# Kernel tuning notes

Measured on AMD Instinct MI355X. Metric: run time of the kernel, lower is better.

## Reference

```python
import jax, jax.numpy as jnp
import numpy as np

B, N_C, N_F = 2, 16384, 65536          # batch, coarse nodes, fine (up_nodes)
C_IN, C_OUT = 128, 128
E_C, E_F = 65536, 262144               # coarse / fine edge counts


def _mlp_params(key, cin, cout):
    # 2-layer MLP (Linear-ReLU-Linear) + LayerNorm, torch default uniform init
    k1, k2 = jax.random.split(key)
    s1 = 1.0 / np.sqrt(2 * cin)
    s2 = 1.0 / np.sqrt(cout)
    W1 = jax.random.uniform(k1, (2 * cin, cout), minval=-s1, maxval=s1, dtype=jnp.float32)
    W2 = jax.random.uniform(k2, (cout, cout), minval=-s2, maxval=s2, dtype=jnp.float32)
    return (W1, jnp.zeros((cout,), jnp.float32), W2, jnp.zeros((cout,), jnp.float32),
            jnp.ones((cout,), jnp.float32), jnp.zeros((cout,), jnp.float32))


def setup_inputs() -> dict:
    key = jax.random.key(0)
    rng = np.random.default_rng(0)
    x = jax.random.normal(jax.random.fold_in(key, 1), (B, N_C, C_IN), dtype=jnp.float32)
    # sorted unique unpool indices (m_id)
    idx = jnp.asarray(np.sort(rng.choice(N_F, N_C, replace=False)).astype(np.int64))
    ei_c = jnp.asarray(rng.integers(0, N_C, size=(2, E_C)).astype(np.int64))
    ei_f = jnp.asarray(rng.integers(0, N_F, size=(2, E_F)).astype(np.int64))
    d = {"x": x, "idx": idx, "ei_c": ei_c, "ei_f": ei_f}
    for pre, k, cin, cout in (("s", 2, C_IN, C_OUT), ("a", 3, C_IN, C_OUT // 2), ("b", 4, C_OUT // 2, C_OUT)):
        W1, b1, W2, b2, g, bt = _mlp_params(jax.random.fold_in(key, k), cin, cout)
        d.update({pre + "W1": W1, pre + "b1": b1, pre + "W2": W2, pre + "b2": b2, pre + "g": g, pre + "bt": bt})
    return d


def _unpool(x, idx, n):
    # scatter coarse features into a zero-filled fine array (Unpool module)
    return jnp.zeros((x.shape[0], n, x.shape[-1]), x.dtype).at[:, idx].set(x)


def _edgeconv(x, ei, W1, b1, W2, b2, g, bt, n):
    # EdgeConv: aggregate_sum over edges of MLP([x_i, x_j - x_i]) + LayerNorm
    src, dst = ei[0], ei[1]
    xd = x[:, dst]                                   # [B,E,cin] gather at target
    feat = jnp.concatenate([xd, x[:, src] - xd], axis=-1)  # [B,E,2*cin]
    h = jax.nn.relu(feat @ W1 + b1) @ W2 + b2        # [B,E,cout]
    mu = jnp.mean(h, axis=-1, keepdims=True)
    var = jnp.var(h, axis=-1, keepdims=True)
    h = (h - mu) * jax.lax.rsqrt(var + 1e-5) * g + bt
    return jax.vmap(lambda hb: jax.ops.segment_sum(hb, dst, num_segments=n))(h)


def reference(x, idx, ei_c, ei_f,
              sW1, sb1, sW2, sb2, sg, sbt,
              aW1, ab1, aW2, ab2, ag, abt,
              bW1, bb1, bW2, bb2, bg, bbt):
    # skip branch: unpool then EdgeConv cin->cout on fine graph
    skip = _edgeconv(_unpool(x, idx, N_F), ei_f, sW1, sb1, sW2, sb2, sg, sbt, N_F)
    # main branch: EdgeConv cin->cout/2 on coarse, unpool, EdgeConv cout/2->cout on fine
    h = _edgeconv(x, ei_c, aW1, ab1, aW2, ab2, ag, abt, N_C)
    h = _edgeconv(_unpool(h, idx, N_F), ei_f, bW1, bb1, bW2, bb2, bg, bbt, N_F)
    return jax.nn.leaky_relu(h + skip, 0.01)
```

## Files before the change

### kernel.cpp

```cpp
#include <hip/hip_runtime.h>

typedef _Float16 half8  __attribute__((ext_vector_type(8)));
typedef _Float16 half4v __attribute__((ext_vector_type(4)));
typedef _Float16 half2v __attribute__((ext_vector_type(2)));
typedef float    f32x4  __attribute__((ext_vector_type(4)));
typedef float    f32x2  __attribute__((ext_vector_type(2)));
typedef int      i32x4  __attribute__((ext_vector_type(4)));

#define NB 2
#define N_C 16384
#define N_F 65536
#define E_C 65536
#define E_F 262144

#define INV4  ((size_t)N_F / 4)
#define CNT4  ((size_t)(N_F + N_C) / 4)

__global__ void clear_small(int* __restrict__ inv, int* __restrict__ cnt) {
    size_t i = (size_t)blockIdx.x * 256 + threadIdx.x;
    const i32x4 z = {0, 0, 0, 0};
    const i32x4 m1 = {-1, -1, -1, -1};
    if (i < INV4) ((i32x4*)inv)[i] = m1;
    else if (i < INV4 + CNT4) ((i32x4*)cnt)[i - INV4] = z;
}

__device__ inline void swizzle_dev(const float* __restrict__ W, _Float16* __restrict__ Ws,
                                   int N, int o) {
    int j = o & 7;
    int lane = (o >> 3) & 63;
    int frag = o >> 9;
    int ntiles = N >> 4;
    int nt = frag % ntiles;
    int kt = frag / ntiles;
    int k = kt * 32 + (lane >> 4) * 8 + j;
    int n = nt * 16 + (lane & 15);
    Ws[o] = (_Float16)W[k * N + n];
}

__device__ inline void swz_node(const float* __restrict__ W, _Float16* __restrict__ Ws,
                                int CIN, int COUT, int o) {
    int j = o & 7;
    int lane = (o >> 3) & 63;
    int frag = o >> 9;
    int N2 = 2 * COUT;
    int ntiles = N2 >> 4;
    int nt = frag % ntiles;
    int kt = frag / ntiles;
    int k = kt * 32 + (lane >> 4) * 8 + j;
    int n = nt * 16 + (lane & 15);
    float v = (n < COUT) ? W[k * COUT + n] - W[(k + CIN) * COUT + n]
                         : W[(k + CIN) * COUT + (n - COUT)];
    Ws[o] = (_Float16)v;
}

__global__ void setup_all(const int* __restrict__ idx, int* __restrict__ inv,
                          const float* sW1, const float* sW2, const float* aW1,
                          const float* aW2, const float* bW1, const float* bW2,
                          const float* sb1, const float* ab1, const float* bb1,
                          _Float16* sW1n, _Float16* sW2s, _Float16* aW1n,
                          _Float16* aW2s, _Float16* bW1n, _Float16* bW2s,
                          _Float16* b1h,
                          const int* __restrict__ ei_f, const int* __restrict__ ei_c,
                          int* __restrict__ cnt) {
    const int bb = blockIdx.x, t = threadIdx.x;
    if (bb < 64) {
        int i = bb * 256 + t;
        inv[idx[i]] = i;
    } else if (bb < 192) {
        swz_node(sW1, sW1n, 128, 128, (bb - 64) * 256 + t);
    } else if (bb < 256) {
        swizzle_dev(sW2, sW2s, 128, (bb - 192) * 256 + t);
    } else if (bb < 320) {
        swz_node(aW1, aW1n, 128, 64, (bb - 256) * 256 + t);
    } else if (bb < 336) {
        swizzle_dev(aW2, aW2s, 64, (bb - 320) * 256 + t);
    } else if (bb < 400) {
        swz_node(bW1, bW1n, 64, 128, (bb - 336) * 256 + t);
    } else if (bb < 464) {
        swizzle_dev(bW2, bW2s, 128, (bb - 400) * 256 + t);
    } else if (bb < 466) {
        int i = (bb - 464) * 256 + t;
        if (i < 128) b1h[i] = (_Float16)sb1[i];
        else if (i < 192) b1h[i] = (_Float16)ab1[i - 128];
        else if (i < 320) b1h[i] = (_Float16)bb1[i - 192];
    } else if (bb < 1490) {
        int e = (bb - 466) * 256 + t;
        atomicAdd(&cnt[ei_f[E_F + e]], 1);
    } else {
        int e = (bb - 1490) * 256 + t;
        atomicAdd(&cnt[N_F + ei_c[E_C + e]], 1);
    }
}

__global__ void scan1(const int* __restrict__ cnt, int* __restrict__ csum) {
    __shared__ int red[4];
    int v = cnt[blockIdx.x * 256 + threadIdx.x];
    #pragma unroll
    for (int off = 32; off >= 1; off >>= 1) v += __shfl_xor(v, off, 64);
    if ((threadIdx.x & 63) == 0) red[threadIdx.x >> 6] = v;
    __syncthreads();
    if (threadIdx.x == 0) csum[blockIdx.x] = red[0] + red[1] + red[2] + red[3];
}

__global__ void scan2(const int* __restrict__ csum, int* __restrict__ cbase) {
    __shared__ int buf[256];
    const int t = threadIdx.x;
    int v = csum[t];
    buf[t] = v;
    __syncthreads();
    for (int off = 1; off < 256; off <<= 1) {
        int u = (t >= off) ? buf[t - off] : 0;
        __syncthreads();
        buf[t] += u;
        __syncthreads();
    }
    cbase[t] = buf[t] - v;
    __syncthreads();
    int v2 = (t < 64) ? csum[256 + t] : 0;
    buf[t] = v2;
    __syncthreads();
    for (int off = 1; off < 64; off <<= 1) {
        int u = (t >= off) ? buf[t - off] : 0;
        __syncthreads();
        buf[t] += u;
        __syncthreads();
    }
    if (t < 64) cbase[256 + t] = buf[t] - v2;
}

__global__ void scan3(const int* __restrict__ cnt, const int* __restrict__ cbase,
                      int* __restrict__ cursor) {
    __shared__ int buf[256];
    const int t = threadIdx.x, bb = blockIdx.x;
    int v = cnt[bb * 256 + t];
    buf[t] = v;
    __syncthreads();
    for (int off = 1; off < 256; off <<= 1) {
        int u = (t >= off) ? buf[t - off] : 0;
        __syncthreads();
        buf[t] += u;
        __syncthreads();
    }
    cursor[bb * 256 + t] = cbase[bb] + buf[t] - v;
}

__global__ void scatter2(const int* __restrict__ ei_f, const int* __restrict__ ei_c,
                         int* __restrict__ cursor,
                         int* __restrict__ perm_f, int* __restrict__ perm_c) {
    const int bb = blockIdx.x, t = threadIdx.x;
    if (bb < 1024) {
        int e = bb * 256 + t;
        int d = ei_f[E_F + e];
        int p = atomicAdd(&cursor[d], 1);
        perm_f[p] = e;
    } else {
        int e = (bb - 1024) * 256 + t;
        int d = ei_c[E_C + e];
        int p = atomicAdd(&cursor[N_F + d], 1);
        perm_c[p] = e;
    }
}

__global__ void zero_flag(const int* __restrict__ cnt, const int* __restrict__ cursor,
                          unsigned char* __restrict__ flagF,
                          float* __restrict__ out, float* __restrict__ h_a) {
    const int d = blockIdx.x * 256 + threadIdx.x;
    const f32x4 z = {0.f, 0.f, 0.f, 0.f};
    if (d < N_F) {
        const int deg = cnt[d];
        const int end = cursor[d];
        const int start = end - deg;
        const bool pred = (deg == 0) || ((start >> 5) != ((end - 1) >> 5));
        flagF[d] = pred ? 1 : 0;
        if (pred) {
            f32x4* r0 = (f32x4*)(out + (size_t)d * 128);
            f32x4* r1 = (f32x4*)(out + ((size_t)N_F + d) * 128);
            #pragma unroll
            for (int i = 0; i < 32; ++i) { r0[i] = z; r1[i] = z; }
        }
    } else if (d < N_F + N_C) {
        const int dc = d - N_F;
        const int deg = cnt[d];
        const int end = cursor[d];
        const int start = end - deg;
        const bool pred = (deg == 0) || ((start >> 4) != ((end - 1) >> 4));
        if (pred) {
            f32x4* r0 = (f32x4*)(h_a + (size_t)dc * 64);
            f32x4* r1 = (f32x4*)(h_a + ((size_t)N_C + dc) * 64);
            #pragma unroll
            for (int i = 0; i < 16; ++i) { r0[i] = z; r1[i] = z; }
        }
    }
}

template <int CIN, int COUT>
__launch_bounds__(256, 4) __global__
void node_gemm(const float* __restrict__ x, const _Float16* __restrict__ W1n,
               const float* __restrict__ b1, _Float16* __restrict__ P) {
    constexpr int N2 = 2 * COUT;
    constexpr int FP = CIN + 8;
    constexpr int P2 = N2 + 8;
    constexpr int NPW = N2 / 4;
    constexpr int NT = NPW / 16;
    constexpr int RH = (64 * FP > 64 * P2) ? 64 * FP : 64 * P2;

    __shared__ __align__(16) _Float16 L[RH];
    const int t = threadIdx.x;
    const size_t r0 = (size_t)blockIdx.x * 64;

    {
        const int m = t >> 2, l4 = t & 3;
        const float* src = x + (r0 + m) * CIN + l4 * (CIN / 4);
        #pragma unroll
        for (int i = 0; i < CIN / 16; ++i) {
            f32x4 v = *(const f32x4*)(src + i * 4);
            half4v h;
            #pragma unroll
            for (int c = 0; c < 4; ++c) h[c] = (_Float16)v[c];
            *(half4v*)(L + m * FP + l4 * (CIN / 4) + i * 4) = h;
        }
    }
    __syncthreads();

    const int wv = t >> 6, lane = t & 63;
    const int q = lane >> 4, lm = lane & 15;
    const int n0 = wv * NPW;
    const f32x4 zero4 = {0.f, 0.f, 0.f, 0.f};

    f32x4 acc[4][NT];
    #pragma unroll
    for (int mt = 0; mt < 4; ++mt)
        #pragma unroll
        for (int nt = 0; nt < NT; ++nt) acc[mt][nt] = zero4;

    #pragma unroll
    for (int kt = 0; kt < CIN / 32; ++kt) {
        half8 a[4];
        #pragma unroll
        for (int mt = 0; mt < 4; ++mt)
            a[mt] = *(const half8*)(L + (mt * 16 + lm) * FP + kt * 32 + q * 8);
        #pragma unroll
        for (int nt = 0; nt < NT; ++nt) {
            half8 bf = *(const half8*)(W1n + ((size_t)(kt * (N2 / 16) + wv * NT + nt) * 64 + lane) * 8);
            #pragma unroll
            for (int mt = 0; mt < 4; ++mt)
                acc[mt][nt] = __builtin_amdgcn_mfma_f32_16x16x32_f16(a[mt], bf, acc[mt][nt], 0, 0, 0);
        }
    }
    __syncthreads();

    #pragma unroll
    for (int nt = 0; nt < NT; ++nt) {
        const int col = n0 + nt * 16 + lm;
        const float bv = (col < COUT) ? b1[col] : 0.f;
        #pragma unroll
        for (int mt = 0; mt < 4; ++mt)
            #pragma unroll
            for (int r = 0; r < 4; ++r)
                L[(mt * 16 + q * 4 + r) * P2 + col] = (_Float16)(acc[mt][nt][r] + bv);
    }
    __syncthreads();

    constexpr int CH = 64 * N2 / 8;
    for (int i = t; i < CH; i += 256) {
        int row = i / (N2 / 8), c8 = i % (N2 / 8);
        *(half8*)(P + (r0 + row) * N2 + c8 * 8) = *(const half8*)(L + row * P2 + c8 * 8);
    }
}

__device__ inline half8 relu8(half8 h) {
#if __has_builtin(__builtin_elementwise_max)
    half8 z = {};
    return __builtin_elementwise_max(h, z);
#else
    #pragma unroll
    for (int i = 0; i < 8; ++i) h[i] = h[i] > (_Float16)0 ? h[i] : (_Float16)0;
    return h;
#endif
}

template <int COUT, bool FRESH>
__launch_bounds__(256, 8) __global__
void edge2_mfma(const _Float16* __restrict__ P, int ps,
                const int* __restrict__ inv,
                const int* __restrict__ ei, const int* __restrict__ perm, int E,
                const _Float16* __restrict__ W2s, const float* __restrict__ b2,
                const float* __restrict__ g, const float* __restrict__ bt,
                const _Float16* __restrict__ b1h,
                float* __restrict__ dest, int bs_out) {
    constexpr int HPITCH = COUT + 8;
    constexpr int NPW = COUT / 4;
    constexpr int NT = NPW / 16;

    __shared__ __align__(16) _Float16 region[64 * HPITCH];
    __shared__ int dstl[64];
    __shared__ int dpnL[2];
    __shared__ float muL[64];
    __shared__ float rsL[64];

    _Float16* h1L = region;
    _Float16* vnL = region;

    const int t = threadIdx.x;
    const int eb = blockIdx.x * 64;
    const int b = eb / E;
    const int e0 = eb - b * E;

    {
        if (t == 0) dpnL[0] = (e0 > 0) ? ei[E + perm[e0 - 1]] : -2;
        else if (t == 1) dpnL[1] = (e0 + 64 < E) ? ei[E + perm[e0 + 64]] : -2;
        const int m = t >> 2, l4 = t & 3;
        const int edge = perm[e0 + m];
        int s = ei[edge], d = ei[E + edge];
        if (l4 == 0) dstl[m] = d;
        int si = s, di = d;
        if (inv) { si = inv[s]; di = inv[d]; }
        const _Float16* pb = P + (size_t)b * ps;
        const _Float16* ub = (di >= 0) ? pb + (size_t)di * (2 * COUT) : b1h;
        const _Float16* vb = pb + (size_t)(si >= 0 ? si : 0) * (2 * COUT) + COUT;
        constexpr int CPT = COUT / 4;
        const int c0 = l4 * CPT;
        #pragma unroll
        for (int i = 0; i < CPT / 8; ++i) {
            half8 u = *(const half8*)(ub + c0 + i * 8);
            half8 v = {};
            if (si >= 0) v = *(const half8*)(vb + c0 + i * 8);
            *(half8*)(h1L + m * HPITCH + c0 + i * 8) = relu8(u + v);
        }
    }
    __syncthreads();

    const int wv = t >> 6, lane = t & 63;
    const int q = lane >> 4, lm = lane & 15;
    const int n0 = wv * NPW;
    const f32x4 zero4 = {0.f, 0.f, 0.f, 0.f};

    f32x4 acc[4][NT];
    #pragma unroll
    for (int mt = 0; mt < 4; ++mt)
        #pragma unroll
        for (int nt = 0; nt < NT; ++nt) acc[mt][nt] = zero4;

    #pragma unroll
    for (int kt = 0; kt < COUT / 32; ++kt) {
        half8 a[4];
        #pragma unroll
        for (int mt = 0; mt < 4; ++mt)
            a[mt] = *(const half8*)(h1L + (mt * 16 + lm) * HPITCH + kt * 32 + q * 8);
        #pragma unroll
        for (int nt = 0; nt < NT; ++nt) {
            half8 bf = *(const half8*)(W2s + ((size_t)(kt * (COUT / 16) + wv * NT + nt) * 64 + lane) * 8);
            #pragma unroll
            for (int mt = 0; mt < 4; ++mt)
                acc[mt][nt] = __builtin_amdgcn_mfma_f32_16x16x32_f16(a[mt], bf, acc[mt][nt], 0, 0, 0);
        }
    }
    __syncthreads();

    #pragma unroll
    for (int nt = 0; nt < NT; ++nt) {
        const float b2v = b2[n0 + nt * 16 + lm];
        #pragma unroll
        for (int mt = 0; mt < 4; ++mt)
            #pragma unroll
            for (int r = 0; r < 4; ++r)
                vnL[(mt * 16 + q * 4 + r) * HPITCH + n0 + nt * 16 + lm] =
                    (_Float16)(acc[mt][nt][r] + b2v);
    }
    __syncthreads();

    {
        const int m = t >> 2, p = t & 3;
        constexpr int CPT = COUT / 4;
        float s = 0.f, s2 = 0.f;
        #pragma unroll
        for (int c = 0; c < CPT / 8; ++c) {
            half8 h8 = *(const half8*)(vnL + m * HPITCH + p * CPT + c * 8);
            #pragma unroll
            for (int j = 0; j < 8; ++j) {
                float v = (float)h8[j];
                s += v;
                s2 += v * v;
            }
        }
        s += __shfl_xor(s, 1, 64);  s2 += __shfl_xor(s2, 1, 64);
        s += __shfl_xor(s, 2, 64);  s2 += __shfl_xor(s2, 2, 64);
        if (p == 0) {
            float mu = s * (1.f / COUT);
            muL[m] = mu;
            rsL[m] = rsqrtf(s2 * (1.f / COUT) - mu * mu + 1e-5f);
        }
    }
    __syncthreads();

    {
        constexpr int CG = COUT / 64;
        constexpr int W  = 4 / CG;
        constexpr int RW = 64 / W;
        const int wv2 = t >> 6, l2 = t & 63;
        const int cg = wv2 % CG;
        const int h  = wv2 / CG;
        const int c  = cg * 64 + l2;
        const int r0 = h * RW;
        const float gv = g[c], bv = bt[c];
        float* const ob = dest + (size_t)b * bs_out + c;
        int dcur = dstl[r0];
        const int dprev = (r0 == 0) ? dpnL[0] : dstl[r0 - 1];
        bool bflag = (dcur == dprev);
        float rs = 0.f;
        #pragma unroll
        for (int i = 0; i < RW; ++i) {
            const int m = r0 + i;
            const float v = (float)vnL[m * HPITCH + c];
            rs += (v - muL[m]) * rsL[m] * gv + bv;
            const int dnxt = (i == RW - 1)
                               ? ((r0 + RW == 64) ? dpnL[1] : dstl[r0 + RW])
                               : dstl[m + 1];
            if (dnxt != dcur) {
                if (!FRESH || bflag) atomicAdd(ob + (size_t)dcur * COUT, rs);
                else ob[(size_t)dcur * COUT] = rs;
                rs = 0.f; dcur = dnxt; bflag = false;
            } else if (i == RW - 1) {
                atomicAdd(ob + (size_t)dcur * COUT, rs);
            }
        }
    }
}

__launch_bounds__(256, 4) __global__
void edge2_dual(const _Float16* __restrict__ Ps, const _Float16* __restrict__ Pb,
                const int* __restrict__ inv,
                const int* __restrict__ ei, const int* __restrict__ perm,
                const _Float16* __restrict__ W2sS, const float* __restrict__ b2s,
                const float* __restrict__ gS, const float* __restrict__ btS,
                const _Float16* __restrict__ W2sB, const float* __restrict__ b2b,
                const float* __restrict__ gB, const float* __restrict__ btB,
                const _Float16* __restrict__ b1hS, const _Float16* __restrict__ b1hB,
                float* __restrict__ out) {
    constexpr int E = E_F;
    constexpr int HP = 136;

    __shared__ __align__(16) _Float16 regS[64 * HP];
    __shared__ __align__(16) _Float16 regB[64 * HP];
    __shared__ int dstl[64];
    __shared__ int dpn[2];
    __shared__ float muS[64], rsS[64], muB[64], rsB[64];

    const int t = threadIdx.x;
    const int eb = blockIdx.x * 64;
    const int b = eb / E;
    const int e0 = eb - b * E;

    {
        if (t == 0) dpn[0] = (e0 > 0) ? ei[E + perm[e0 - 1]] : -2;
        else if (t == 1) dpn[1] = (e0 + 64 < E) ? ei[E + perm[e0 + 64]] : -2;
        const int m = t >> 2, l4 = t & 3;
        const int edge = perm[e0 + m];
        const int s = ei[edge], d = ei[E + edge];
        if (l4 == 0) dstl[m] = d;
        const int si = inv[s], di = inv[d];
        const size_t pofs = (size_t)b * ((size_t)N_C * 256);
        const _Float16* ubS = (di >= 0) ? Ps + pofs + (size_t)di * 256 : b1hS;
        const _Float16* ubB = (di >= 0) ? Pb + pofs + (size_t)di * 256 : b1hB;
        const size_t so = (size_t)(si >= 0 ? si : 0) * 256 + 128;
        const _Float16* vbS = Ps + pofs + so;
        const _Float16* vbB = Pb + pofs + so;
        const int c0 = l4 * 32;
        #pragma unroll
        for (int i = 0; i < 4; ++i) {
            half8 uS = *(const half8*)(ubS + c0 + i * 8);
            half8 uB = *(const half8*)(ubB + c0 + i * 8);
            half8 vS = {}, vB = {};
            if (si >= 0) {
                vS = *(const half8*)(vbS + c0 + i * 8);
                vB = *(const half8*)(vbB + c0 + i * 8);
            }
            *(half8*)(regS + m * HP + c0 + i * 8) = relu8(uS + vS);
            *(half8*)(regB + m * HP + c0 + i * 8) = relu8(uB + vB);
        }
    }
    __syncthreads();

    const int wv = t >> 6, lane = t & 63;
    const int q = lane >> 4, lm = lane & 15;
    const int n0 = wv * 32;
    const f32x4 zero4 = {0.f, 0.f, 0.f, 0.f};

    f32x4 accS[4][2], accB[4][2];
    #pragma unroll
    for (int mt = 0; mt < 4; ++mt)
        #pragma unroll
        for (int nt = 0; nt < 2; ++nt) { accS[mt][nt] = zero4; accB[mt][nt] = zero4; }

    #pragma unroll
    for (int kt = 0; kt < 4; ++kt) {
        half8 aS[4], aB[4];
        #pragma unroll
        for (int mt = 0; mt < 4; ++mt) {
            aS[mt] = *(const half8*)(regS + (mt * 16 + lm) * HP + kt * 32 + q * 8);
            aB[mt] = *(const half8*)(regB + (mt * 16 + lm) * HP + kt * 32 + q * 8);
        }
        #pragma unroll
        for (int nt = 0; nt < 2; ++nt) {
            half8 bS = *(const half8*)(W2sS + ((size_t)(kt * 8 + wv * 2 + nt) * 64 + lane) * 8);
            half8 bB = *(const half8*)(W2sB + ((size_t)(kt * 8 + wv * 2 + nt) * 64 + lane) * 8);
            #pragma unroll
            for (int mt = 0; mt < 4; ++mt) {
                accS[mt][nt] = __builtin_amdgcn_mfma_f32_16x16x32_f16(aS[mt], bS, accS[mt][nt], 0, 0, 0);
                accB[mt][nt] = __builtin_amdgcn_mfma_f32_16x16x32_f16(aB[mt], bB, accB[mt][nt], 0, 0, 0);
            }
        }
    }
    __syncthreads();

    #pragma unroll
    for (int nt = 0; nt < 2; ++nt) {
        const float b2vS = b2s[n0 + nt * 16 + lm];
        const float b2vB = b2b[n0 + nt * 16 + lm];
        #pragma unroll
        for (int mt = 0; mt < 4; ++mt)
            #pragma unroll
            for (int r = 0; r < 4; ++r) {
                const int row = mt * 16 + q * 4 + r;
                regS[row * HP + n0 + nt * 16 + lm] = (_Float16)(accS[mt][nt][r] + b2vS);
                regB[row * HP + n0 + nt * 16 + lm] = (_Float16)(accB[mt][nt][r] + b2vB);
            }
    }
    __syncthreads();

    {
        const int m = t >> 2, p = t & 3;
        float sS = 0.f, s2S = 0.f, sB = 0.f, s2B = 0.f;
        #pragma unroll
        for (int c8 = 0; c8 < 4; ++c8) {
            half8 hS = *(const half8*)(regS + m * HP + p * 32 + c8 * 8);
            half8 hB = *(const half8*)(regB + m * HP + p * 32 + c8 * 8);
            #pragma unroll
            for (int j = 0; j < 8; ++j) {
                float a = (float)hS[j]; sS += a; s2S += a * a;
                float c = (float)hB[j]; sB += c; s2B += c * c;
            }
        }
        sS += __shfl_xor(sS, 1, 64);  s2S += __shfl_xor(s2S, 1, 64);
        sS += __shfl_xor(sS, 2, 64);  s2S += __shfl_xor(s2S, 2, 64);
        sB += __shfl_xor(sB, 1, 64);  s2B += __shfl_xor(s2B, 1, 64);
        sB += __shfl_xor(sB, 2, 64);  s2B += __shfl_xor(s2B, 2, 64);
        if (p == 0) {
            float mS = sS * (1.f / 128.f);
            muS[m] = mS;
            rsS[m] = rsqrtf(s2S * (1.f / 128.f) - mS * mS + 1e-5f);
            float mB = sB * (1.f / 128.f);
            muB[m] = mB;
            rsB[m] = rsqrtf(s2B * (1.f / 128.f) - mB * mB + 1e-5f);
        }
    }
    __syncthreads();

    {
        const int wv2 = t >> 6, l2 = t & 63;
        const int cg = wv2 & 1;
        const int h  = wv2 >> 1;
        const int c  = cg * 64 + l2;
        const int r0 = h * 32;
        const float gs = gS[c], bs_ = btS[c];
        const float gb = gB[c], bb_ = btB[c];
        float* const ob = out + (size_t)b * ((size_t)N_F * 128) + c;
        int dcur = dstl[r0];
        const int dprev = (r0 == 0) ? dpn[0] : dstl[r0 - 1];
        bool bflag = (dcur == dprev);
        float rs = 0.f;
        #pragma unroll
        for (int i = 0; i < 32; ++i) {
            const int m = r0 + i;
            const float vs_ = (float)regS[m * HP + c];
            const float vb_ = (float)regB[m * HP + c];
            rs += (vs_ - muS[m]) * rsS[m] * gs + bs_
                + (vb_ - muB[m]) * rsB[m] * gb + bb_;
            const int dnxt = (i == 31)
                               ? ((r0 + 32 == 64) ? dpn[1] : dstl[r0 + 32])
                               : dstl[m + 1];
            if (dnxt != dcur) {
                if (bflag) {
                    atomicAdd(ob + (size_t)dcur * 128, rs);
                } else {
                    float v = rs > 0.f ? rs : 0.01f * rs;
                    ob[(size_t)dcur * 128] = v;
                }
                rs = 0.f; dcur = dnxt; bflag = false;
            } else if (i == 31) {
                atomicAdd(ob + (size_t)dcur * 128, rs);
            }
        }
    }
}

__global__ void leaky_fix(float* __restrict__ out, const unsigned char* __restrict__ flagF) {
    const size_t i = (size_t)blockIdx.x * 256 + threadIdx.x;
    if (i >= (size_t)NB * N_F * 32) return;
    const int d = (int)((i >> 5) & (N_F - 1));
    if (!flagF[d]) return;
    f32x4 v = ((f32x4*)out)[i];
    #pragma unroll
    for (int c = 0; c < 4; ++c) v[c] = v[c] > 0.f ? v[c] : 0.01f * v[c];
    ((f32x4*)out)[i] = v;
}

extern "C" void kernel_launch(void* const* d_in, const int* in_sizes, int n_in,
                              void* d_out, int out_size, void* d_ws, size_t ws_size,
                              hipStream_t stream) {
    const float* x    = (const float*)d_in[0];
    const int*   idx  = (const int*)d_in[1];
    const int*   ei_c = (const int*)d_in[2];
    const int*   ei_f = (const int*)d_in[3];
    const float* sW1 = (const float*)d_in[4];
    const float* sb1 = (const float*)d_in[5];
    const float* sW2 = (const float*)d_in[6];
    const float* sb2 = (const float*)d_in[7];
    const float* sg  = (const float*)d_in[8];
    const float* sbt = (const float*)d_in[9];
    const float* aW1 = (const float*)d_in[10];
    const float* ab1 = (const float*)d_in[11];
    const float* aW2 = (const float*)d_in[12];
    const float* ab2 = (const float*)d_in[13];
    const float* ag  = (const float*)d_in[14];
    const float* abt = (const float*)d_in[15];
    const float* bW1 = (const float*)d_in[16];
    const float* bb1 = (const float*)d_in[17];
    const float* bW2 = (const float*)d_in[18];
    const float* bb2 = (const float*)d_in[19];
    const float* bg  = (const float*)d_in[20];
    const float* bbt = (const float*)d_in[21];

    float* out = (float*)d_out;

    char* ws = (char*)d_ws;
    int*   inv    = (int*)ws;                                ws += (size_t)N_F * 4;
    float* h_a    = (float*)ws;                              ws += (size_t)NB * N_C * 64 * 4;
    int*   perm_f = (int*)ws;                                ws += (size_t)E_F * 4;
    int*   perm_c = (int*)ws;                                ws += (size_t)E_C * 4;
    int*   cnt    = (int*)ws;                                ws += (size_t)(N_F + N_C) * 4;
    int*   cursor = (int*)ws;                                ws += (size_t)(N_F + N_C) * 4;
    int*   csum   = (int*)ws;                                ws += 320 * 4;
    int*   cbase  = (int*)ws;                                ws += 320 * 4;
    _Float16* sW1n = (_Float16*)ws;                          ws += (size_t)128 * 256 * 2;
    _Float16* sW2s = (_Float16*)ws;                          ws += (size_t)128 * 128 * 2;
    _Float16* aW1n = (_Float16*)ws;                          ws += (size_t)128 * 128 * 2;
    _Float16* aW2s = (_Float16*)ws;                          ws += (size_t)64 * 64 * 2;
    _Float16* bW1n = (_Float16*)ws;                          ws += (size_t)64 * 256 * 2;
    _Float16* bW2s = (_Float16*)ws;                          ws += (size_t)128 * 128 * 2;
    _Float16* b1h  = (_Float16*)ws;                          ws += 1024;
    unsigned char* flagF = (unsigned char*)ws;               ws += (size_t)N_F;
    _Float16* P_s  = (_Float16*)ws;                          ws += (size_t)NB * N_C * 256 * 2;
    _Float16* P_a  = (_Float16*)ws;                          ws += (size_t)NB * N_C * 128 * 2;
    _Float16* P_b  = (_Float16*)ws;                          ws += (size_t)NB * N_C * 256 * 2;

    clear_small<<<(int)((INV4 + CNT4 + 255) / 256), 256, 0, stream>>>(inv, cnt);

    setup_all<<<1746, 256, 0, stream>>>(idx, inv, sW1, sW2, aW1, aW2, bW1, bW2,
                                        sb1, ab1, bb1,
                                        sW1n, sW2s, aW1n, aW2s, bW1n, bW2s, b1h,
                                        ei_f, ei_c, cnt);

    scan1<<<320, 256, 0, stream>>>(cnt, csum);
    scan2<<<1, 256, 0, stream>>>(csum, cbase);
    scan3<<<320, 256, 0, stream>>>(cnt, cbase, cursor);
    scatter2<<<1280, 256, 0, stream>>>(ei_f, ei_c, cursor, perm_f, perm_c);

    zero_flag<<<(N_F + N_C) / 256, 256, 0, stream>>>(cnt, cursor, flagF, out, h_a);

    node_gemm<128, 128><<<NB * N_C / 64, 256, 0, stream>>>(x, sW1n, sb1, P_s);
    node_gemm<128, 64><<<NB * N_C / 64, 256, 0, stream>>>(x, aW1n, ab1, P_a);

    edge2_mfma<64, true><<<NB * E_C / 64, 256, 0, stream>>>(
        P_a, N_C * 128, nullptr, ei_c, perm_c, E_C, aW2s, ab2, ag, abt, b1h + 128, h_a, N_C * 64);

    node_gemm<64, 128><<<NB * N_C / 64, 256, 0, stream>>>(h_a, bW1n, bb1, P_b);

    edge2_dual<<<NB * E_F / 64, 256, 0, stream>>>(
        P_s, P_b, inv, ei_f, perm_f,
        sW2s, sb2, sg, sbt,
        bW2s, bb2, bg, bbt,
        b1h, b1h + 192, out);

    leaky_fix<<<(int)(((size_t)NB * N_F * 32 + 255) / 256), 256, 0, stream>>>(out, flagF);
}
```

Measured before the change: 307.5 us.

## Fuse preprocessing into one cooperative kernel and precompute per-edge index records

```diff
diff --git a/kernel.cpp b/kernel.cpp
--- a/kernel.cpp
+++ b/kernel.cpp
@@ -1,4 +1,7 @@
 #include <hip/hip_runtime.h>
+#include <hip/hip_cooperative_groups.h>
+
+namespace cg = cooperative_groups;
 
 typedef _Float16 half8  __attribute__((ext_vector_type(8)));
 typedef _Float16 half4v __attribute__((ext_vector_type(4)));
@@ -15,14 +18,6 @@
 
 #define INV4  ((size_t)N_F / 4)
 #define CNT4  ((size_t)(N_F + N_C) / 4)
-
-__global__ void clear_small(int* __restrict__ inv, int* __restrict__ cnt) {
-    size_t i = (size_t)blockIdx.x * 256 + threadIdx.x;
-    const i32x4 z = {0, 0, 0, 0};
-    const i32x4 m1 = {-1, -1, -1, -1};
-    if (i < INV4) ((i32x4*)inv)[i] = m1;
-    else if (i < INV4 + CNT4) ((i32x4*)cnt)[i - INV4] = z;
-}
 
 __device__ inline void swizzle_dev(const float* __restrict__ W, _Float16* __restrict__ Ws,
                                    int N, int o) {
@@ -53,160 +48,164 @@
     Ws[o] = (_Float16)v;
 }
 
-__global__ void setup_all(const int* __restrict__ idx, int* __restrict__ inv,
-                          const float* sW1, const float* sW2, const float* aW1,
-                          const float* aW2, const float* bW1, const float* bW2,
-                          const float* sb1, const float* ab1, const float* bb1,
-                          _Float16* sW1n, _Float16* sW2s, _Float16* aW1n,
-                          _Float16* aW2s, _Float16* bW1n, _Float16* bW2s,
-                          _Float16* b1h,
-                          const int* __restrict__ ei_f, const int* __restrict__ ei_c,
-                          int* __restrict__ cnt) {
+struct PrepArgs {
+    const int* idx; int* inv;
+    const float *sW1, *sW2, *aW1, *aW2, *bW1, *bW2;
+    const float *sb1, *ab1, *bb1;
+    _Float16 *sW1n, *sW2s, *aW1n, *aW2s, *bW1n, *bW2s, *b1h;
+    const int *ei_f, *ei_c;
+    int *cnt, *csum, *cbase, *cursor;
+    i32x4 *ef_info, *ec_info;
+    unsigned char* flagF;
+    float *out, *h_a;
+};
+
+__global__ void prep(PrepArgs A) {
+    cg::grid_group grid = cg::this_grid();
+    __shared__ int sbuf[256];
     const int bb = blockIdx.x, t = threadIdx.x;
+
+    {
+        size_t i = (size_t)bb * 256 + t;
+        const i32x4 z = {0, 0, 0, 0};
+        const i32x4 m1 = {-1, -1, -1, -1};
+        if (i < INV4) ((i32x4*)A.inv)[i] = m1;
+        else if (i < INV4 + CNT4) ((i32x4*)A.cnt)[i - INV4] = z;
+    }
+    grid.sync();
+
     if (bb < 64) {
         int i = bb * 256 + t;
-        inv[idx[i]] = i;
+        A.inv[A.idx[i]] = i;
     } else if (bb < 192) {
-        swz_node(sW1, sW1n, 128, 128, (bb - 64) * 256 + t);
+        swz_node(A.sW1, A.sW1n, 128, 128, (bb - 64) * 256 + t);
     } else if (bb < 256) {
-        swizzle_dev(sW2, sW2s, 128, (bb - 192) * 256 + t);
+        swizzle_dev(A.sW2, A.sW2s, 128, (bb - 192) * 256 + t);
     } else if (bb < 320) {
-        swz_node(aW1, aW1n, 128, 64, (bb - 256) * 256 + t);
+        swz_node(A.aW1, A.aW1n, 128, 64, (bb - 256) * 256 + t);
     } else if (bb < 336) {
-        swizzle_dev(aW2, aW2s, 64, (bb - 320) * 256 + t);
+        swizzle_dev(A.aW2, A.aW2s, 64, (bb - 320) * 256 + t);
     } else if (bb < 400) {
-        swz_node(bW1, bW1n, 64, 128, (bb - 336) * 256 + t);
+        swz_node(A.bW1, A.bW1n, 64, 128, (bb - 336) * 256 + t);
     } else if (bb < 464) {
-        swizzle_dev(bW2, bW2s, 128, (bb - 400) * 256 + t);
+        swizzle_dev(A.bW2, A.bW2s, 128, (bb - 400) * 256 + t);
     } else if (bb < 466) {
         int i = (bb - 464) * 256 + t;
-        if (i < 128) b1h[i] = (_Float16)sb1[i];
-        else if (i < 192) b1h[i] = (_Float16)ab1[i - 128];
-        else if (i < 320) b1h[i] = (_Float16)bb1[i - 192];
+        if (i < 128) A.b1h[i] = (_Float16)A.sb1[i];
+        else if (i < 192) A.b1h[i] = (_Float16)A.ab1[i - 128];
+        else if (i < 320) A.b1h[i] = (_Float16)A.bb1[i - 192];
     } else if (bb < 1490) {
         int e = (bb - 466) * 256 + t;
-        atomicAdd(&cnt[ei_f[E_F + e]], 1);
+        atomicAdd(&A.cnt[A.ei_f[E_F + e]], 1);
     } else {
         int e = (bb - 1490) * 256 + t;
-        atomicAdd(&cnt[N_F + ei_c[E_C + e]], 1);
-    }
-}
-
-__global__ void scan1(const int* __restrict__ cnt, int* __restrict__ csum) {
-    __shared__ int red[4];
-    int v = cnt[blockIdx.x * 256 + threadIdx.x];
-    #pragma unroll
-    for (int off = 32; off >= 1; off >>= 1) v += __shfl_xor(v, off, 64);
-    if ((threadIdx.x & 63) == 0) red[threadIdx.x >> 6] = v;
-    __syncthreads();
-    if (threadIdx.x == 0) csum[blockIdx.x] = red[0] + red[1] + red[2] + red[3];
-}
-
-__global__ void scan2(const int* __restrict__ csum, int* __restrict__ cbase) {
-    __shared__ int buf[256];
-    const int t = threadIdx.x;
-    int v = csum[t];
-    buf[t] = v;
-    __syncthreads();
-    for (int off = 1; off < 256; off <<= 1) {
-        int u = (t >= off) ? buf[t - off] : 0;
+        atomicAdd(&A.cnt[N_F + A.ei_c[E_C + e]], 1);
+    }
+    grid.sync();
+
+    if (bb < 320) {
+        int v = A.cnt[bb * 256 + t];
+        #pragma unroll
+        for (int off = 32; off >= 1; off >>= 1) v += __shfl_xor(v, off, 64);
+        if ((t & 63) == 0) sbuf[t >> 6] = v;
         __syncthreads();
-        buf[t] += u;
+        if (t == 0) A.csum[bb] = sbuf[0] + sbuf[1] + sbuf[2] + sbuf[3];
+    }
+    grid.sync();
+
+    if (bb == 0) {
+        int v = A.csum[t];
+        sbuf[t] = v;
         __syncthreads();
-    }
-    cbase[t] = buf[t] - v;
-    __syncthreads();
-    int v2 = (t < 64) ? csum[256 + t] : 0;
-    buf[t] = v2;
-    __syncthreads();
-    for (int off = 1; off < 64; off <<= 1) {
-        int u = (t >= off) ? buf[t - off] : 0;
+        for (int off = 1; off < 256; off <<= 1) {
+            int u = (t >= off) ? sbuf[t - off] : 0;
+            __syncthreads();
+            sbuf[t] += u;
+            __syncthreads();
+        }
+        A.cbase[t] = sbuf[t] - v;
         __syncthreads();
-        buf[t] += u;
+        int v2 = (t < 64) ? A.csum[256 + t] : 0;
+        sbuf[t] = v2;
         __syncthreads();
-    }
-    if (t < 64) cbase[256 + t] = buf[t] - v2;
-}
-
-__global__ void scan3(const int* __restrict__ cnt, const int* __restrict__ cbase,
-                      int* __restrict__ cursor) {
-    __shared__ int buf[256];
-    const int t = threadIdx.x, bb = blockIdx.x;
-    int v = cnt[bb * 256 + t];
-    buf[t] = v;
-    __syncthreads();
-    for (int off = 1; off < 256; off <<= 1) {
-        int u = (t >= off) ? buf[t - off] : 0;
+        for (int off = 1; off < 64; off <<= 1) {
+            int u = (t >= off) ? sbuf[t - off] : 0;
+            __syncthreads();
+            sbuf[t] += u;
+            __syncthreads();
+        }
+        if (t < 64) A.cbase[256 + t] = sbuf[t] - v2;
+    }
+    grid.sync();
+
+    if (bb < 320) {
+        const int d = bb * 256 + t;
+        int v = A.cnt[d];
+        sbuf[t] = v;
         __syncthreads();
-        buf[t] += u;
-        __syncthreads();
-    }
-    cursor[bb * 256 + t] = cbase[bb] + buf[t] - v;
-}
-
-__global__ void scatter2(const int* __restrict__ ei_f, const int* __restrict__ ei_c,
-                         int* __restrict__ cursor,
-                         int* __restrict__ perm_f, int* __restrict__ perm_c) {
-    const int bb = blockIdx.x, t = threadIdx.x;
+        for (int off = 1; off < 256; off <<= 1) {
+            int u = (t >= off) ? sbuf[t - off] : 0;
+            __syncthreads();
+            sbuf[t] += u;
+            __syncthreads();
+        }
+        const int start = A.cbase[bb] + sbuf[t] - v;
+        A.cursor[d] = start;
+        const int deg = v;
+        const int end = start + deg;
+        const f32x4 z = {0.f, 0.f, 0.f, 0.f};
+        if (d < N_F) {
+            const bool pred = (deg == 0) || ((start >> 5) != ((end - 1) >> 5));
+            A.flagF[d] = pred ? 1 : 0;
+            if (pred) {
+                f32x4* r0 = (f32x4*)(A.out + (size_t)d * 128);
+                f32x4* r1 = (f32x4*)(A.out + ((size_t)N_F + d) * 128);
+                #pragma unroll
+                for (int i = 0; i < 32; ++i) { r0[i] = z; r1[i] = z; }
+            }
+        } else {
+            const int dc = d - N_F;
+            const bool pred = (deg == 0) || ((start >> 4) != ((end - 1) >> 4));
+            if (pred) {
+                f32x4* r0 = (f32x4*)(A.h_a + (size_t)dc * 64);
+                f32x4* r1 = (f32x4*)(A.h_a + ((size_t)N_C + dc) * 64);
+                #pragma unroll
+                for (int i = 0; i < 16; ++i) { r0[i] = z; r1[i] = z; }
+            }
+        }
+    }
+    grid.sync();
+
     if (bb < 1024) {
         int e = bb * 256 + t;
-        int d = ei_f[E_F + e];
-        int p = atomicAdd(&cursor[d], 1);
-        perm_f[p] = e;
-    } else {
+        int s_ = A.ei_f[e];
+        int d_ = A.ei_f[E_F + e];
+        int p = atomicAdd(&A.cursor[d_], 1);
+        i32x4 rec;
+        rec.x = A.inv[s_]; rec.y = A.inv[d_]; rec.z = d_; rec.w = 0;
+        A.ef_info[p] = rec;
+    } else if (bb < 1280) {
         int e = (bb - 1024) * 256 + t;
-        int d = ei_c[E_C + e];
-        int p = atomicAdd(&cursor[N_F + d], 1);
-        perm_c[p] = e;
-    }
-}
-
-__global__ void zero_flag(const int* __restrict__ cnt, const int* __restrict__ cursor,
-                          unsigned char* __restrict__ flagF,
-                          float* __restrict__ out, float* __restrict__ h_a) {
-    const int d = blockIdx.x * 256 + threadIdx.x;
-    const f32x4 z = {0.f, 0.f, 0.f, 0.f};
-    if (d < N_F) {
-        const int deg = cnt[d];
-        const int end = cursor[d];
-        const int start = end - deg;
-        const bool pred = (deg == 0) || ((start >> 5) != ((end - 1) >> 5));
-        flagF[d] = pred ? 1 : 0;
-        if (pred) {
-            f32x4* r0 = (f32x4*)(out + (size_t)d * 128);
-            f32x4* r1 = (f32x4*)(out + ((size_t)N_F + d) * 128);
-            #pragma unroll
-            for (int i = 0; i < 32; ++i) { r0[i] = z; r1[i] = z; }
-        }
-    } else if (d < N_F + N_C) {
-        const int dc = d - N_F;
-        const int deg = cnt[d];
-        const int end = cursor[d];
-        const int start = end - deg;
-        const bool pred = (deg == 0) || ((start >> 4) != ((end - 1) >> 4));
-        if (pred) {
-            f32x4* r0 = (f32x4*)(h_a + (size_t)dc * 64);
-            f32x4* r1 = (f32x4*)(h_a + ((size_t)N_C + dc) * 64);
-            #pragma unroll
-            for (int i = 0; i < 16; ++i) { r0[i] = z; r1[i] = z; }
-        }
+        int s_ = A.ei_c[e];
+        int d_ = A.ei_c[E_C + e];
+        int p = atomicAdd(&A.cursor[N_F + d_], 1);
+        i32x4 rec;
+        rec.x = s_; rec.y = d_; rec.z = d_; rec.w = 0;
+        A.ec_info[p] = rec;
     }
 }
 
 template <int CIN, int COUT>
-__launch_bounds__(256, 4) __global__
-void node_gemm(const float* __restrict__ x, const _Float16* __restrict__ W1n,
-               const float* __restrict__ b1, _Float16* __restrict__ P) {
+__device__ void node_gemm_body(const float* __restrict__ x, const _Float16* __restrict__ W1n,
+                               const float* __restrict__ b1, _Float16* __restrict__ P,
+                               _Float16* L, int blk, int t) {
     constexpr int N2 = 2 * COUT;
     constexpr int FP = CIN + 8;
     constexpr int P2 = N2 + 8;
     constexpr int NPW = N2 / 4;
     constexpr int NT = NPW / 16;
-    constexpr int RH = (64 * FP > 64 * P2) ? 64 * FP : 64 * P2;
-
-    __shared__ __align__(16) _Float16 L[RH];
-    const int t = threadIdx.x;
-    const size_t r0 = (size_t)blockIdx.x * 64;
+
+    const size_t r0 = (size_t)blk * 64;
 
     {
         const int m = t >> 2, l4 = t & 3;
@@ -266,6 +265,26 @@
         int row = i / (N2 / 8), c8 = i % (N2 / 8);
         *(half8*)(P + (r0 + row) * N2 + c8 * 8) = *(const half8*)(L + row * P2 + c8 * 8);
     }
+}
+
+__launch_bounds__(256, 4) __global__
+void node_sa(const float* __restrict__ x,
+             const _Float16* __restrict__ sW1n, const float* __restrict__ sb1, _Float16* __restrict__ Ps,
+             const _Float16* __restrict__ aW1n, const float* __restrict__ ab1, _Float16* __restrict__ Pa) {
+    __shared__ __align__(16) _Float16 L[16896];
+    const int t = threadIdx.x;
+    if (blockIdx.x < NB * N_C / 64)
+        node_gemm_body<128, 128>(x, sW1n, sb1, Ps, L, blockIdx.x, t);
+    else
+        node_gemm_body<128, 64>(x, aW1n, ab1, Pa, L, blockIdx.x - NB * N_C / 64, t);
+}
+
+template <int CIN, int COUT>
+__launch_bounds__(256, 4) __global__
+void node_gemm(const float* __restrict__ x, const _Float16* __restrict__ W1n,
+               const float* __restrict__ b1, _Float16* __restrict__ P) {
+    __shared__ __align__(16) _Float16 L[16896];
+    node_gemm_body<CIN, COUT>(x, W1n, b1, P, L, blockIdx.x, threadIdx.x);
 }
 
 __device__ inline half8 relu8(half8 h) {
@@ -282,8 +301,7 @@
 template <int COUT, bool FRESH>
 __launch_bounds__(256, 8) __global__
 void edge2_mfma(const _Float16* __restrict__ P, int ps,
-                const int* __restrict__ inv,
-                const int* __restrict__ ei, const int* __restrict__ perm, int E,
+                const i32x4* __restrict__ einfo, int E,
                 const _Float16* __restrict__ W2s, const float* __restrict__ b2,
                 const float* __restrict__ g, const float* __restrict__ bt,
                 const _Float16* __restrict__ b1h,
@@ -307,14 +325,12 @@
     const int e0 = eb - b * E;
 
     {
-        if (t == 0) dpnL[0] = (e0 > 0) ? ei[E + perm[e0 - 1]] : -2;
-        else if (t == 1) dpnL[1] = (e0 + 64 < E) ? ei[E + perm[e0 + 64]] : -2;
+        if (t == 0) dpnL[0] = (e0 > 0) ? einfo[e0 - 1].z : -2;
+        else if (t == 1) dpnL[1] = (e0 + 64 < E) ? einfo[e0 + 64].z : -2;
         const int m = t >> 2, l4 = t & 3;
-        const int edge = perm[e0 + m];
-        int s = ei[edge], d = ei[E + edge];
-        if (l4 == 0) dstl[m] = d;
-        int si = s, di = d;
-        if (inv) { si = inv[s]; di = inv[d]; }
+        const i32x4 rec = einfo[e0 + m];
+        const int si = rec.x, di = rec.y;
+        if (l4 == 0) dstl[m] = rec.z;
         const _Float16* pb = P + (size_t)b * ps;
         const _Float16* ub = (di >= 0) ? pb + (size_t)di * (2 * COUT) : b1h;
         const _Float16* vb = pb + (size_t)(si >= 0 ? si : 0) * (2 * COUT) + COUT;
@@ -429,8 +445,7 @@
 
 __launch_bounds__(256, 4) __global__
 void edge2_dual(const _Float16* __restrict__ Ps, const _Float16* __restrict__ Pb,
-                const int* __restrict__ inv,
-                const int* __restrict__ ei, const int* __restrict__ perm,
+                const i32x4* __restrict__ einfo,
                 const _Float16* __restrict__ W2sS, const float* __restrict__ b2s,
                 const float* __restrict__ gS, const float* __restrict__ btS,
                 const _Float16* __restrict__ W2sB, const float* __restrict__ b2b,
@@ -439,12 +454,16 @@
                 float* __restrict__ out) {
     constexpr int E = E_F;
     constexpr int HP = 136;
-
-    __shared__ __align__(16) _Float16 regS[64 * HP];
-    __shared__ __align__(16) _Float16 regB[64 * HP];
+    constexpr int IP = 264;
+
+    __shared__ __align__(16) _Float16 region[2 * 64 * HP];
     __shared__ int dstl[64];
     __shared__ int dpn[2];
-    __shared__ float muS[64], rsS[64], muB[64], rsB[64];
+    __shared__ f32x4 stat4[64];
+
+    _Float16* h1S = region;
+    _Float16* h1B = region + 64 * HP;
+    _Float16* vnI = region;
 
     const int t = threadIdx.x;
     const int eb = blockIdx.x * 64;
@@ -452,13 +471,12 @@
     const int e0 = eb - b * E;
 
     {
-        if (t == 0) dpn[0] = (e0 > 0) ? ei[E + perm[e0 - 1]] : -2;
-        else if (t == 1) dpn[1] = (e0 + 64 < E) ? ei[E + perm[e0 + 64]] : -2;
+        if (t == 0) dpn[0] = (e0 > 0) ? einfo[e0 - 1].z : -2;
+        else if (t == 1) dpn[1] = (e0 + 64 < E) ? einfo[e0 + 64].z : -2;
         const int m = t >> 2, l4 = t & 3;
-        const int edge = perm[e0 + m];
-        const int s = ei[edge], d = ei[E + edge];
-        if (l4 == 0) dstl[m] = d;
-        const int si = inv[s], di = inv[d];
+        const i32x4 rec = einfo[e0 + m];
+        const int si = rec.x, di = rec.y;
+        if (l4 == 0) dstl[m] = rec.z;
         const size_t pofs = (size_t)b * ((size_t)N_C * 256);
         const _Float16* ubS = (di >= 0) ? Ps + pofs + (size_t)di * 256 : b1hS;
         const _Float16* ubB = (di >= 0) ? Pb + pofs + (size_t)di * 256 : b1hB;
@@ -475,8 +493,8 @@
                 vS = *(const half8*)(vbS + c0 + i * 8);
                 vB = *(const half8*)(vbB + c0 + i * 8);
             }
-            *(half8*)(regS + m * HP + c0 + i * 8) = relu8(uS + vS);
-            *(half8*)(regB + m * HP + c0 + i * 8) = relu8(uB + vB);
+            *(half8*)(h1S + m * HP + c0 + i * 8) = relu8(uS + vS);
+            *(half8*)(h1B + m * HP + c0 + i * 8) = relu8(uB + vB);
         }
     }
     __syncthreads();
@@ -497,8 +515,8 @@
         half8 aS[4], aB[4];
         #pragma unroll
         for (int mt = 0; mt < 4; ++mt) {
-            aS[mt] = *(const half8*)(regS + (mt * 16 + lm) * HP + kt * 32 + q * 8);
-            aB[mt] = *(const half8*)(regB + (mt * 16 + lm) * HP + kt * 32 + q * 8);
+            aS[mt] = *(const half8*)(h1S + (mt * 16 + lm) * HP + kt * 32 + q * 8);
+            aB[mt] = *(const half8*)(h1B + (mt * 16 + lm) * HP + kt * 32 + q * 8);
         }
         #pragma unroll
         for (int nt = 0; nt < 2; ++nt) {
@@ -515,15 +533,18 @@
 
     #pragma unroll
     for (int nt = 0; nt < 2; ++nt) {
-        const float b2vS = b2s[n0 + nt * 16 + lm];
-        const float b2vB = b2b[n0 + nt * 16 + lm];
+        const int col = n0 + nt * 16 + lm;
+        const float b2vS = b2s[col];
+        const float b2vB = b2b[col];
         #pragma unroll
         for (int mt = 0; mt < 4; ++mt)
             #pragma unroll
             for (int r = 0; r < 4; ++r) {
                 const int row = mt * 16 + q * 4 + r;
-                regS[row * HP + n0 + nt * 16 + lm] = (_Float16)(accS[mt][nt][r] + b2vS);
-                regB[row * HP + n0 + nt * 16 + lm] = (_Float16)(accB[mt][nt][r] + b2vB);
+                half2v pk;
+                pk[0] = (_Float16)(accS[mt][nt][r] + b2vS);
+                pk[1] = (_Float16)(accB[mt][nt][r] + b2vB);
+                *(half2v*)(vnI + row * IP + col * 2) = pk;
             }
     }
     __syncthreads();
@@ -532,13 +553,12 @@
         const int m = t >> 2, p = t & 3;
         float sS = 0.f, s2S = 0.f, sB = 0.f, s2B = 0.f;
         #pragma unroll
-        for (int c8 = 0; c8 < 4; ++c8) {
-            half8 hS = *(const half8*)(regS + m * HP + p * 32 + c8 * 8);
-            half8 hB = *(const half8*)(regB + m * HP + p * 32 + c8 * 8);
-            #pragma unroll
-            for (int j = 0; j < 8; ++j) {
-                float a = (float)hS[j]; sS += a; s2S += a * a;
-                float c = (float)hB[j]; sB += c; s2B += c * c;
+        for (int k = 0; k < 8; ++k) {
+            half8 h8 = *(const half8*)(vnI + m * IP + p * 64 + k * 8);
+            #pragma unroll
+            for (int j = 0; j < 8; j += 2) {
+                float a = (float)h8[j];     sS += a; s2S += a * a;
+                float c = (float)h8[j + 1]; sB += c; s2B += c * c;
             }
         }
         sS += __shfl_xor(sS, 1, 64);  s2S += __shfl_xor(s2S, 1, 64);
@@ -546,12 +566,13 @@
         sB += __shfl_xor(sB, 1, 64);  s2B += __shfl_xor(s2B, 1, 64);
         sB += __shfl_xor(sB, 2, 64);  s2B += __shfl_xor(s2B, 2, 64);
         if (p == 0) {
-            float mS = sS * (1.f / 128.f);
-            muS[m] = mS;
-            rsS[m] = rsqrtf(s2S * (1.f / 128.f) - mS * mS + 1e-5f);
-            float mB = sB * (1.f / 128.f);
-            muB[m] = mB;
-            rsB[m] = rsqrtf(s2B * (1.f / 128.f) - mB * mB + 1e-5f);
+            const float mS = sS * (1.f / 128.f);
+            const float rS = rsqrtf(s2S * (1.f / 128.f) - mS * mS + 1e-5f);
+            const float mB = sB * (1.f / 128.f);
+            const float rB = rsqrtf(s2B * (1.f / 128.f) - mB * mB + 1e-5f);
+            f32x4 st;
+            st[0] = rS; st[1] = -mS * rS; st[2] = rB; st[3] = -mB * rB;
+            stat4[m] = st;
         }
     }
     __syncthreads();
@@ -562,8 +583,8 @@
         const int h  = wv2 >> 1;
         const int c  = cg * 64 + l2;
         const int r0 = h * 32;
-        const float gs = gS[c], bs_ = btS[c];
-        const float gb = gB[c], bb_ = btB[c];
+        const float gS_ = gS[c], gB_ = gB[c];
+        const float bsum = btS[c] + btB[c];
         float* const ob = out + (size_t)b * ((size_t)N_F * 128) + c;
         int dcur = dstl[r0];
         const int dprev = (r0 == 0) ? dpn[0] : dstl[r0 - 1];
@@ -572,10 +593,10 @@
         #pragma unroll
         for (int i = 0; i < 32; ++i) {
             const int m = r0 + i;
-            const float vs_ = (float)regS[m * HP + c];
-            const float vb_ = (float)regB[m * HP + c];
-            rs += (vs_ - muS[m]) * rsS[m] * gs + bs_
-                + (vb_ - muB[m]) * rsB[m] * gb + bb_;
+            const half2v v2 = *(const half2v*)(vnI + m * IP + c * 2);
+            const f32x4 st = stat4[m];
+            rs += fmaf((float)v2[0], st[0], st[1]) * gS_
+                + fmaf((float)v2[1], st[2], st[3]) * gB_ + bsum;
             const int dnxt = (i == 31)
                                ? ((r0 + 32 == 64) ? dpn[1] : dstl[r0 + 32])
                                : dstl[m + 1];
@@ -636,12 +657,12 @@
     char* ws = (char*)d_ws;
     int*   inv    = (int*)ws;                                ws += (size_t)N_F * 4;
     float* h_a    = (float*)ws;                              ws += (size_t)NB * N_C * 64 * 4;
-    int*   perm_f = (int*)ws;                                ws += (size_t)E_F * 4;
-    int*   perm_c = (int*)ws;                                ws += (size_t)E_C * 4;
     int*   cnt    = (int*)ws;                                ws += (size_t)(N_F + N_C) * 4;
     int*   cursor = (int*)ws;                                ws += (size_t)(N_F + N_C) * 4;
     int*   csum   = (int*)ws;                                ws += 320 * 4;
     int*   cbase  = (int*)ws;                                ws += 320 * 4;
+    i32x4* ef_info = (i32x4*)ws;                             ws += (size_t)E_F * 16;
+    i32x4* ec_info = (i32x4*)ws;                             ws += (size_t)E_C * 16;
     _Float16* sW1n = (_Float16*)ws;                          ws += (size_t)128 * 256 * 2;
     _Float16* sW2s = (_Float16*)ws;                          ws += (size_t)128 * 128 * 2;
     _Float16* aW1n = (_Float16*)ws;                          ws += (size_t)128 * 128 * 2;
@@ -654,30 +675,28 @@
     _Float16* P_a  = (_Float16*)ws;                          ws += (size_t)NB * N_C * 128 * 2;
     _Float16* P_b  = (_Float16*)ws;                          ws += (size_t)NB * N_C * 256 * 2;
 
-    clear_small<<<(int)((INV4 + CNT4 + 255) / 256), 256, 0, stream>>>(inv, cnt);
-
-    setup_all<<<1746, 256, 0, stream>>>(idx, inv, sW1, sW2, aW1, aW2, bW1, bW2,
-                                        sb1, ab1, bb1,
-                                        sW1n, sW2s, aW1n, aW2s, bW1n, bW2s, b1h,
-                                        ei_f, ei_c, cnt);
-
-    scan1<<<320, 256, 0, stream>>>(cnt, csum);
-    scan2<<<1, 256, 0, stream>>>(csum, cbase);
-    scan3<<<320, 256, 0, stream>>>(cnt, cbase, cursor);
-    scatter2<<<1280, 256, 0, stream>>>(ei_f, ei_c, cursor, perm_f, perm_c);
-
-    zero_flag<<<(N_F + N_C) / 256, 256, 0, stream>>>(cnt, cursor, flagF, out, h_a);
-
-    node_gemm<128, 128><<<NB * N_C / 64, 256, 0, stream>>>(x, sW1n, sb1, P_s);
-    node_gemm<128, 64><<<NB * N_C / 64, 256, 0, stream>>>(x, aW1n, ab1, P_a);
+    PrepArgs pa;
+    pa.idx = idx; pa.inv = inv;
+    pa.sW1 = sW1; pa.sW2 = sW2; pa.aW1 = aW1; pa.aW2 = aW2; pa.bW1 = bW1; pa.bW2 = bW2;
+    pa.sb1 = sb1; pa.ab1 = ab1; pa.bb1 = bb1;
+    pa.sW1n = sW1n; pa.sW2s = sW2s; pa.aW1n = aW1n; pa.aW2s = aW2s; pa.bW1n = bW1n; pa.bW2s = bW2s;
+    pa.b1h = b1h;
+    pa.ei_f = ei_f; pa.ei_c = ei_c;
+    pa.cnt = cnt; pa.csum = csum; pa.cbase = cbase; pa.cursor = cursor;
+    pa.ef_info = ef_info; pa.ec_info = ec_info;
+    pa.flagF = flagF; pa.out = out; pa.h_a = h_a;
+    void* kargs[] = { &pa };
+    hipLaunchCooperativeKernel((void*)prep, dim3(1746), dim3(256), kargs, 0, stream);
+
+    node_sa<<<2 * (NB * N_C / 64), 256, 0, stream>>>(x, sW1n, sb1, P_s, aW1n, ab1, P_a);
 
     edge2_mfma<64, true><<<NB * E_C / 64, 256, 0, stream>>>(
-        P_a, N_C * 128, nullptr, ei_c, perm_c, E_C, aW2s, ab2, ag, abt, b1h + 128, h_a, N_C * 64);
+        P_a, N_C * 128, ec_info, E_C, aW2s, ab2, ag, abt, b1h + 128, h_a, N_C * 64);
 
     node_gemm<64, 128><<<NB * N_C / 64, 256, 0, stream>>>(h_a, bW1n, bb1, P_b);
 
     edge2_dual<<<NB * E_F / 64, 256, 0, stream>>>(
-        P_s, P_b, inv, ei_f, perm_f,
+        P_s, P_b, ef_info,
         sW2s, sb2, sg, sbt,
         bW2s, bb2, bg, bbt,
         b1h, b1h + 192, out);
```

New measurement: 1.200 ms. 290% more time.
